# Optimization experiments

Measured on AMD Instinct MI355X. Metric: run time of the kernel, lower is better.

The kernel has to match this reference:

```python
import jax, jax.numpy as jnp
import numpy as np

V, E, H = 32000, 512, 1024
B, T = 32, 48
PAD = 0


def setup_inputs() -> dict:
    key = jax.random.key(0)
    ks = jax.random.split(key, 9)
    s = 0.05
    emb = jax.random.normal(ks[0], (V, E), jnp.float32) * s
    emb = emb.at[PAD].set(0.0)  # padding_idx row is zero in nn.Embedding
    return {
        "initial_hidden_state": jax.random.normal(ks[1], (B, H), jnp.float32),
        "target_sequence": jax.random.randint(ks[2], (B, T), 0, V),
        "emb": emb,
        "W_ih": jax.random.normal(ks[3], (3 * H, E), jnp.float32) * s,  # [r;z;n] input weights
        "W_hh": jax.random.normal(ks[4], (3 * H, H), jnp.float32) * s,
        "b_ih": jax.random.normal(ks[5], (3 * H,), jnp.float32) * s,
        "b_hh": jax.random.normal(ks[6], (3 * H,), jnp.float32) * s,
        "W_cls": jax.random.normal(ks[7], (V, H), jnp.float32) * s,
        "b_cls": jax.random.normal(ks[8], (V,), jnp.float32) * s,
    }


def _decode(initial_hidden_state, target_sequence, emb, W_ih, W_hh, b_ih, b_hh, W_cls, b_cls):
    # teacher forcing: sample_probability = 0.0 -> use_sample False
    idx_t = target_sequence.T  # [T, B]

    def step(h, y_idx):
        x = emb[y_idx]                                 # [B, E] embedding gather
        gi = x @ W_ih.T + b_ih                         # [B, 3H]
        gh = h @ W_hh.T + b_hh                         # [B, 3H]
        i_r, i_z, i_n = jnp.split(gi, 3, axis=-1)
        h_r, h_z, h_n = jnp.split(gh, 3, axis=-1)
        r = jax.nn.sigmoid(i_r + h_r)
        z = jax.nn.sigmoid(i_z + h_z)
        n = jnp.tanh(i_n + r * h_n)
        h_new = (1.0 - z) * n + z * h                  # torch GRUCell update
        score = h_new @ W_cls.T + b_cls                # [B, V]
        return h_new, score

    _, scores = jax.lax.scan(step, initial_hidden_state, idx_t)  # [T, B, V]
    return jnp.transpose(scores, (1, 0, 2))                      # [B, T, V]


def reference(initial_hidden_state, target_sequence, emb, W_ih, W_hh, b_ih, b_hh, W_cls, b_cls):
    return _decode(initial_hidden_state, target_sequence, emb, W_ih, W_hh, b_ih, b_hh, W_cls, b_cls)
```

## Files before the change

### kernel.cpp

```cpp
#include <hip/hip_runtime.h>
#include <hip/hip_bf16.h>

typedef __attribute__((ext_vector_type(8))) short short8;
typedef __attribute__((ext_vector_type(4))) float f32x4;
typedef __attribute__((ext_vector_type(4))) unsigned int u32x4;

#define T_STEPS 48
#define BATCH 32
#define EDIM 512
#define HDIM 1024
#define VOCAB 32000
#define GRU_BLOCKS 64
#define JPB 16
#define SENT 0x7FFF7FFFu
#define N_TILES 750
#define CNT_STRIDE 16
#define EARLY_WORKERS 128

#define HS_T_STRIDE 16384

__device__ __forceinline__ unsigned short f2bf(float f) {
    __hip_bfloat16 h = __float2bfloat16(f);
    return *reinterpret_cast<unsigned short*>(&h);
}
__device__ __forceinline__ float bf2f(unsigned short u) {
    union { unsigned int i; float f; } v;
    v.i = ((unsigned int)u) << 16;
    return v.f;
}

typedef __attribute__((address_space(1))) const void GAS;
typedef __attribute__((address_space(3))) void LAS;
__device__ __forceinline__ void gload_lds16(const unsigned short* g, unsigned short* l) {
    __builtin_amdgcn_global_load_lds((GAS*)g, (LAS*)(unsigned)(uintptr_t)l, 16, 0, 0);
}

__device__ __forceinline__ void store16_coh(unsigned int* p, u32x4 v) {
    asm volatile("global_store_dwordx4 %0, %1, off sc0 sc1"
                 :: "v"((unsigned long long)(uintptr_t)p), "v"(v) : "memory");
}

__global__ __launch_bounds__(256) void prep_kernel(
    const float* __restrict__ h0, const int* __restrict__ tseq,
    const float* __restrict__ emb, const float* __restrict__ w_ih,
    const float* __restrict__ w_hh, const float* __restrict__ w_cls,
    unsigned short* __restrict__ wcls_bf, unsigned short* __restrict__ wih_bf,
    unsigned short* __restrict__ whh_bf, unsigned short* __restrict__ x_bf,
    unsigned int* __restrict__ hs32, unsigned int* __restrict__ cnt8)
{
    const long R0 = (long)VOCAB * HDIM / 4;
    const long R1 = (long)3 * HDIM * EDIM / 4;
    const long R2 = (long)3 * HDIM * HDIM / 4;
    const long R3 = (long)T_STEPS * BATCH * EDIM / 4;
    const long R4 = (long)HS_T_STRIDE;
    const long R5 = (long)T_STEPS * HS_T_STRIDE / 4;
    const long R6 = 512;
    const long total = R0 + R1 + R2 + R3 + R4 + R5 + R6;

    for (long i = (long)blockIdx.x * blockDim.x + threadIdx.x; i < total;
         i += (long)gridDim.x * blockDim.x) {
        if (i < R0) {
            float4 v = reinterpret_cast<const float4*>(w_cls)[i];
            ushort4 u = { f2bf(v.x), f2bf(v.y), f2bf(v.z), f2bf(v.w) };
            *reinterpret_cast<ushort4*>(wcls_bf + i * 4) = u;
        } else if (i < R0 + R1) {
            long j = i - R0;
            float4 v = reinterpret_cast<const float4*>(w_ih)[j];
            ushort4 u = { f2bf(v.x), f2bf(v.y), f2bf(v.z), f2bf(v.w) };
            *reinterpret_cast<ushort4*>(wih_bf + j * 4) = u;
        } else if (i < R0 + R1 + R2) {
            long j = i - R0 - R1;
            float4 v = reinterpret_cast<const float4*>(w_hh)[j];
            ushort4 u = { f2bf(v.x), f2bf(v.y), f2bf(v.z), f2bf(v.w) };
            *reinterpret_cast<ushort4*>(whh_bf + j * 4) = u;
        } else if (i < R0 + R1 + R2 + R3) {
            long j = i - R0 - R1 - R2;
            int m = (int)(j >> 7);
            int kk4 = (int)(j & 127);
            int t = m >> 5, b = m & 31;
            int tok = tseq[b * T_STEPS + t];
            float4 v = reinterpret_cast<const float4*>(emb)[(long)tok * (EDIM / 4) + kk4];
            ushort4 u = { f2bf(v.x), f2bf(v.y), f2bf(v.z), f2bf(v.w) };
            *reinterpret_cast<ushort4*>(x_bf + (long)m * EDIM + kk4 * 4) = u;
        } else if (i < R0 + R1 + R2 + R3 + R4) {
            long j = i - R0 - R1 - R2 - R3;
            int w = (int)(j >> 5), b = (int)(j & 31);
            unsigned short a = f2bf(h0[b * HDIM + 2 * w]);
            unsigned short c = f2bf(h0[b * HDIM + 2 * w + 1]);
            hs32[j] = (unsigned)a | ((unsigned)c << 16);
        } else if (i < R0 + R1 + R2 + R3 + R4 + R5) {
            long j = i - R0 - R1 - R2 - R3 - R4;
            uint4 s = { SENT, SENT, SENT, SENT };
            reinterpret_cast<uint4*>(hs32 + HS_T_STRIDE)[j] = s;
        } else {
            long j = i - R0 - R1 - R2 - R3 - R4 - R5;
            uint4 z = { 0u, 0u, 0u, 0u };
            reinterpret_cast<uint4*>(cnt8)[j] = z;
        }
    }
}

__global__ __launch_bounds__(256) void gemm_gi(
    const unsigned short* __restrict__ A, const unsigned short* __restrict__ B,
    const float* __restrict__ bias, float* __restrict__ C, int K, int Ntot, int nM)
{
    const int nwg = gridDim.x;
    const int lin = blockIdx.x;
    const int q = nwg >> 3;
    const int wg = (lin & 7) * q + (lin >> 3);
    const int mi = wg % nM, ni = wg / nM;
    const int m0 = mi * 128, n0 = ni * 128;

    const int tid = threadIdx.x;
    const int lane = tid & 63;
    const int wid = tid >> 6;
    const int wr = wid >> 1, wc = wid & 1;

    __shared__ __align__(16) unsigned short As[128 * 32];
    __shared__ __align__(16) unsigned short Bs[128 * 32];

    f32x4 acc[4][4] = {};
    const int NT = K >> 5;
    const int srow = (lane >> 2);
    const int skk = (lane & 3) * 8;

    for (int kt = 0; kt < NT; ++kt) {
        __syncthreads();
        {
            const int kb = kt * 32;
#pragma unroll
            for (int h2 = 0; h2 < 2; ++h2) {
                const int i = wid + h2 * 4;
                const int row = i * 16 + srow;
                gload_lds16(A + (size_t)(m0 + row) * K + kb + skk, As + i * 512);
                gload_lds16(B + (size_t)(n0 + row) * K + kb + skk, Bs + i * 512);
            }
        }
        __syncthreads();

        const int kg = lane >> 4;
        const int l15 = lane & 15;
        short8 af[4], bf[4];
#pragma unroll
        for (int i = 0; i < 4; ++i) {
            af[i] = *(const short8*)(As + ((wr * 64 + i * 16 + l15) * 32 + kg * 8));
            bf[i] = *(const short8*)(Bs + ((wc * 64 + i * 16 + l15) * 32 + kg * 8));
        }
#pragma unroll
        for (int i = 0; i < 4; ++i)
#pragma unroll
            for (int j = 0; j < 4; ++j)
                acc[i][j] = __builtin_amdgcn_mfma_f32_16x16x32_bf16(af[i], bf[j], acc[i][j], 0, 0, 0);
    }

    const int l15 = lane & 15, lhi = lane >> 4;
#pragma unroll
    for (int i = 0; i < 4; ++i)
#pragma unroll
        for (int j = 0; j < 4; ++j) {
            int col = n0 + wc * 64 + j * 16 + l15;
            float bv = bias[col];
#pragma unroll
            for (int q2 = 0; q2 < 4; ++q2) {
                int row = m0 + wr * 64 + i * 16 + lhi * 4 + q2;
                C[(size_t)row * Ntot + col] = acc[i][j][q2] + bv;
            }
        }
}

__global__ __launch_bounds__(512, 1) void fused_kernel(
    unsigned int* __restrict__ hs32, unsigned int* __restrict__ hrow32,
    const unsigned short* __restrict__ whh_bf,
    const float* __restrict__ gi, const float* __restrict__ b_hh,
    const float* __restrict__ h0,
    const unsigned short* __restrict__ wcls_bf, const float* __restrict__ b_cls,
    float* __restrict__ out, unsigned int* __restrict__ cnt8,
    unsigned int* __restrict__ tileq)
{
    __shared__ __align__(16) char smem[124160];
    __shared__ unsigned short Hs[BATCH][JPB];
    __shared__ int sTile;

    const int tid = threadIdx.x;
    const int bid = blockIdx.x;
    const int lane = tid & 63, wid = tid >> 6;
    const int l15 = lane & 15, kg = lane >> 4;

    if (bid < GRU_BLOCKS) {
        unsigned short (*Wl)[1032] = reinterpret_cast<unsigned short (*)[1032]>(smem);
        float (*P)[32][49] = reinterpret_cast<float (*)[32][49]>(smem + 99072);

        const int j0 = bid * JPB;
        for (int c = tid; c < 48 * 128; c += 512) {
            int row = c >> 7, k8 = (c & 127) * 8;
            int g = row >> 4, jj = row & 15;
            *(short8*)&Wl[row][k8] =
                *(const short8*)(whh_bf + (size_t)(g * HDIM + j0 + jj) * HDIM + k8);
        }
        const int b = tid >> 4, jj = tid & 15;
        const int gj = j0 + jj;
        const float bhr = b_hh[gj];
        const float bhz = b_hh[HDIM + gj];
        const float bhn = b_hh[2 * HDIM + gj];
        float hloc = h0[b * HDIM + gj];
        __syncthreads();

        for (int t = 0; t < T_STEPS; ++t) {
            const size_t tb = (size_t)t * HS_T_STRIDE;
            const float* gr = gi + (size_t)(t * BATCH + b) * (3 * HDIM);
            float xr = gr[gj], xz = gr[HDIM + gj], xn = gr[2 * HDIM + gj];

            if (tid < 256) {
                if (t) {
                    const unsigned int* cp = cnt8 + (size_t)t * CNT_STRIDE + 2 * wid;
                    for (;;) {
                        unsigned ok = (lane < 2)
                            ? (__hip_atomic_load(cp + lane, __ATOMIC_RELAXED, __HIP_MEMORY_SCOPE_AGENT) >= 8u ? 1u : 0u)
                            : 1u;
                        if (__all(ok != 0u)) break;
                        __builtin_amdgcn_s_sleep(2);
                    }
                    asm volatile("" ::: "memory");
                }

                const int kq = wid * 256;
                unsigned wv[8][8];
#pragma unroll
                for (int ks = 0; ks < 8; ++ks) {
                    const int wbase = wid * 128 + ks * 16 + kg * 4;
#pragma unroll
                    for (int mi2 = 0; mi2 < 2; ++mi2) {
                        const int bb = mi2 * 16 + l15;
#pragma unroll
                        for (int q = 0; q < 4; ++q)
                            wv[ks][mi2 * 4 + q] = *(const unsigned*)(
                                hs32 + tb + (size_t)(wbase + q) * 32 + bb);
                    }
                }
                for (;;) {
                    int bad = 0;
#pragma unroll
                    for (int ks = 0; ks < 8; ++ks)
#pragma unroll
                        for (int i = 0; i < 8; ++i)
                            bad |= (wv[ks][i] == SENT);
                    if (!__any(bad)) break;
                    __builtin_amdgcn_s_sleep(1);
#pragma unroll
                    for (int ks = 0; ks < 8; ++ks)
#pragma unroll
                        for (int i = 0; i < 8; ++i)
                            if (wv[ks][i] == SENT) {
                                const int mi2 = i >> 2, q = i & 3;
                                wv[ks][i] = __hip_atomic_load(
                                    hs32 + tb + (size_t)(wid * 128 + ks * 16 + kg * 4 + q) * 32 + (mi2 * 16 + l15),
                                    __ATOMIC_RELAXED, __HIP_MEMORY_SCOPE_AGENT);
                            }
                }
                f32x4 acc[2][3] = {};
#pragma unroll
                for (int ks = 0; ks < 8; ++ks) {
                    const int kb = kq + ks * 32 + kg * 8;
                    union U8 { unsigned u[4]; short8 s; };
                    short8 ah[2];
#pragma unroll
                    for (int mi2 = 0; mi2 < 2; ++mi2) {
                        U8 x;
#pragma unroll
                        for (int q = 0; q < 4; ++q) x.u[q] = wv[ks][mi2 * 4 + q];
                        ah[mi2] = x.s;
                    }
#pragma unroll
                    for (int fr = 0; fr < 3; ++fr) {
                        short8 bh = *(const short8*)&Wl[fr * 16 + l15][kb];
#pragma unroll
                        for (int mi2 = 0; mi2 < 2; ++mi2)
                            acc[mi2][fr] = __builtin_amdgcn_mfma_f32_16x16x32_bf16(ah[mi2], bh, acc[mi2][fr], 0, 0, 0);
                    }
                }
#pragma unroll
                for (int mi2 = 0; mi2 < 2; ++mi2)
#pragma unroll
                    for (int fr = 0; fr < 3; ++fr)
#pragma unroll
                        for (int q = 0; q < 4; ++q)
                            P[wid][mi2 * 16 + kg * 4 + q][fr * 16 + l15] = acc[mi2][fr][q];
            }
            __syncthreads();

            {
                float ghr = 0.f, ghz = 0.f, ghn = 0.f;
#pragma unroll
                for (int w = 0; w < 4; ++w) {
                    ghr += P[w][b][jj];
                    ghz += P[w][b][16 + jj];
                    ghn += P[w][b][32 + jj];
                }
                float r = 1.f / (1.f + __expf(-(xr + ghr + bhr)));
                float z = 1.f / (1.f + __expf(-(xz + ghz + bhz)));
                float n = tanhf(xn + r * (ghn + bhn));
                float hnew = (1.f - z) * n + z * hloc;
                hloc = hnew;
                Hs[b][jj] = f2bf(hnew);
            }
            __syncthreads();

            if (tid < 64) {
                const int q = tid >> 3, c = tid & 7;
                u32x4 d;
#pragma unroll
                for (int w2 = 0; w2 < 4; ++w2) {
                    int bb = c * 4 + w2;
                    d[w2] = (unsigned)Hs[bb][2 * q] | ((unsigned)Hs[bb][2 * q + 1] << 16);
                }
                store16_coh(hs32 + (size_t)(t + 1) * HS_T_STRIDE + (size_t)((j0 >> 1) + q) * 32 + c * 4, d);
            } else if (tid < 128) {
                const int i = tid - 64, bb = i >> 1, half = i & 1;
                u32x4 d;
#pragma unroll
                for (int w2 = 0; w2 < 4; ++w2) {
                    int q = half * 4 + w2;
                    d[w2] = (unsigned)Hs[bb][2 * q] | ((unsigned)Hs[bb][2 * q + 1] << 16);
                }
                store16_coh(hrow32 + ((size_t)t * BATCH + bb) * 512 + (j0 >> 1) + half * 4, d);
            }
            __syncthreads();
            if (tid == 0)
                __hip_atomic_fetch_add(cnt8 + (size_t)(t + 1) * CNT_STRIDE + (bid >> 3), 1u,
                                       __ATOMIC_RELAXED, __HIP_MEMORY_SCOPE_AGENT);
        }
    } else if (bid >= GRU_BLOCKS + EARLY_WORKERS) {
        if (wid == 0) {
            const unsigned int* cp = cnt8 + (size_t)T_STEPS * CNT_STRIDE;
            for (;;) {
                unsigned v = (lane < 8)
                    ? __hip_atomic_load(cp + lane, __ATOMIC_RELAXED, __HIP_MEMORY_SCOPE_AGENT)
                    : 8u;
                if (__all(v >= 8u)) break;
                __builtin_amdgcn_s_sleep(64);
            }
        }
        __syncthreads();
    }

    const unsigned short* hrowA = (const unsigned short*)hrow32;
    const int srow = lane >> 2;
    const int skk = (lane & 3) * 8;
    const int wm = wid >> 1, wn = wid & 1;

    unsigned short* As0 = (unsigned short*)(smem);
    unsigned short* Bs0 = (unsigned short*)(smem + 16384);
    unsigned short* As1 = (unsigned short*)(smem + 32768);
    unsigned short* Bs1 = (unsigned short*)(smem + 49152);

    for (;;) {
        __syncthreads();
        if (tid == 0)
            sTile = (int)__hip_atomic_fetch_add(tileq, 1u, __ATOMIC_RELAXED, __HIP_MEMORY_SCOPE_AGENT);
        __syncthreads();
        const int k = sTile;
        if (k >= N_TILES) break;
        const int mi = k / 125, ni = k - mi * 125;
        const int m0 = mi * 256, n0 = ni * 256;

        {
            if (wid == 0) {
                const unsigned int* cp = cnt8 + (size_t)(mi * 8 + 8) * CNT_STRIDE;
                for (;;) {
                    unsigned v = (lane < 8)
                        ? __hip_atomic_load(cp + lane, __ATOMIC_RELAXED, __HIP_MEMORY_SCOPE_AGENT)
                        : 8u;
                    if (__all(v >= 8u)) break;
                    __builtin_amdgcn_s_sleep(32);
                }
            }
            __syncthreads();
            asm volatile("" ::: "memory");
        }

        f32x4 acc[4][8] = {};

#define STAGE(KT, AB, BB)                                                      \
        {                                                                      \
            const int kb = (KT) * 32;                                          \
            _Pragma("unroll")                                                  \
            for (int h2 = 0; h2 < 2; ++h2) {                                   \
                const int i = wid + h2 * 8;                                    \
                const int row = i * 16 + srow;                                 \
                gload_lds16(hrowA + (size_t)(m0 + row) * HDIM + kb + skk, (AB) + i * 512); \
                gload_lds16(wcls_bf + (size_t)(n0 + row) * HDIM + kb + skk, (BB) + i * 512); \
            }                                                                  \
        }
#define COMPUTE(AB, BB)                                                        \
        {                                                                      \
            short8 af[4], bf[8];                                               \
            _Pragma("unroll")                                                  \
            for (int i = 0; i < 4; ++i)                                        \
                af[i] = *(const short8*)((AB) + ((wm * 64 + i * 16 + l15) * 32 + kg * 8)); \
            _Pragma("unroll")                                                  \
            for (int j = 0; j < 8; ++j)                                        \
                bf[j] = *(const short8*)((BB) + ((wn * 128 + j * 16 + l15) * 32 + kg * 8)); \
            _Pragma("unroll")                                                  \
            for (int i = 0; i < 4; ++i)                                        \
                _Pragma("unroll")                                              \
                for (int j = 0; j < 8; ++j)                                    \
                    acc[i][j] = __builtin_amdgcn_mfma_f32_16x16x32_bf16(af[i], bf[j], acc[i][j], 0, 0, 0); \
        }

        STAGE(0, As0, Bs0);
        __syncthreads();
        for (int it = 0; it < 16; ++it) {
            const int kt0 = 2 * it;
            STAGE(kt0 + 1, As1, Bs1);
            COMPUTE(As0, Bs0);
            __syncthreads();
            if (kt0 + 2 < 32) STAGE(kt0 + 2, As0, Bs0);
            COMPUTE(As1, Bs1);
            __syncthreads();
        }
#undef STAGE
#undef COMPUTE

        const int lhi = lane >> 4;
#pragma unroll
        for (int i = 0; i < 4; ++i)
#pragma unroll
            for (int j = 0; j < 8; ++j) {
                int col = n0 + wn * 128 + j * 16 + l15;
                float bv = b_cls[col];
#pragma unroll
                for (int q2 = 0; q2 < 4; ++q2) {
                    int row = m0 + wm * 64 + i * 16 + lhi * 4 + q2;
                    int t = row >> 5, bb = row & 31;
                    __builtin_nontemporal_store(acc[i][j][q2] + bv,
                        &out[(size_t)(bb * T_STEPS + t) * VOCAB + col]);
                }
            }
    }
}

extern "C" void kernel_launch(void* const* d_in, const int* in_sizes, int n_in,
                              void* d_out, int out_size, void* d_ws, size_t ws_size,
                              hipStream_t stream) {
    const float* h0    = (const float*)d_in[0];
    const int*   tseq  = (const int*)d_in[1];
    const float* emb   = (const float*)d_in[2];
    const float* w_ih  = (const float*)d_in[3];
    const float* w_hh  = (const float*)d_in[4];
    const float* b_ih  = (const float*)d_in[5];
    const float* b_hh  = (const float*)d_in[6];
    const float* w_cls = (const float*)d_in[7];
    const float* b_cls = (const float*)d_in[8];
    float* out = (float*)d_out;

    char* w = (char*)d_ws;
    unsigned short* wcls_bf = (unsigned short*)w; w += (size_t)VOCAB * HDIM * 2;
    unsigned short* wih_bf  = (unsigned short*)w; w += (size_t)3 * HDIM * EDIM * 2;
    unsigned short* whh_bf  = (unsigned short*)w; w += (size_t)3 * HDIM * HDIM * 2;
    unsigned short* x_bf    = (unsigned short*)w; w += (size_t)T_STEPS * BATCH * EDIM * 2;
    unsigned int*   hs32    = (unsigned int*)w;   w += (size_t)(T_STEPS + 1) * HS_T_STRIDE * 4;
    unsigned int*   hrow32  = (unsigned int*)w;   w += (size_t)T_STEPS * BATCH * 512 * 4;
    float* gi               = (float*)w;          w += (size_t)T_STEPS * BATCH * 3 * HDIM * 4;
    unsigned int* cnt8      = (unsigned int*)w;   w += 8192;
    unsigned int* tileq     = cnt8 + 1024;

    prep_kernel<<<2048, 256, 0, stream>>>(h0, tseq, emb, w_ih, w_hh, w_cls,
                                          wcls_bf, wih_bf, whh_bf, x_bf, hs32, cnt8);

    gemm_gi<<<(T_STEPS * BATCH / 128) * (3 * HDIM / 128), 256, 0, stream>>>(
        x_bf, wih_bf, b_ih, gi, EDIM, 3 * HDIM, T_STEPS * BATCH / 128);

    fused_kernel<<<256, 512, 0, stream>>>(hs32, hrow32, whh_bf, gi, b_hh, h0,
                                          wcls_bf, b_cls, out, cnt8, tileq);
}
```

Baseline: 345.7 us.

## Split last M-block into half-height tiles to balance classifier GEMM tail

The classifier GEMM's final row block (the last 256 rows of h, which wait on the latest GRU steps) is now covered by 128x256 tiles instead of 256x256 ones, making 250 small tiles after the 625 big ones. The smaller tiles use a separate 4x2 warp layout with their own staging and LDS offsets. This is meant to shrink the tail that runs after the recurrence finishes and spread it over more workgroups. The early-worker count also drops from 128 to 96. The cost is extra code size and more register pressure from two code paths, plus lower per-tile reuse for the last block.

Result: no change. 343.2 us, median of 2 (-0.7%).

```diff
diff --git a/kernel.cpp b/kernel.cpp
--- a/kernel.cpp
+++ b/kernel.cpp
@@ -13,9 +13,10 @@
 #define GRU_BLOCKS 64
 #define JPB 16
 #define SENT 0x7FFF7FFFu
-#define N_TILES 750
+#define N_BIG 625
+#define N_TILES 875
 #define CNT_STRIDE 16
-#define EARLY_WORKERS 128
+#define EARLY_WORKERS 96
 
 #define HS_T_STRIDE 16384
 
@@ -346,12 +347,6 @@
     const unsigned short* hrowA = (const unsigned short*)hrow32;
     const int srow = lane >> 2;
     const int skk = (lane & 3) * 8;
-    const int wm = wid >> 1, wn = wid & 1;
-
-    unsigned short* As0 = (unsigned short*)(smem);
-    unsigned short* Bs0 = (unsigned short*)(smem + 16384);
-    unsigned short* As1 = (unsigned short*)(smem + 32768);
-    unsigned short* Bs1 = (unsigned short*)(smem + 49152);
 
     for (;;) {
         __syncthreads();
@@ -360,8 +355,10 @@
         __syncthreads();
         const int k = sTile;
         if (k >= N_TILES) break;
-        const int mi = k / 125, ni = k - mi * 125;
-        const int m0 = mi * 256, n0 = ni * 256;
+
+        int mi, m0, n0, big;
+        if (k < N_BIG) { mi = k / 125; n0 = (k - mi * 125) * 256; m0 = mi * 256; big = 1; }
+        else { int idx = k - N_BIG; mi = 5; m0 = 1280 + (idx & 1) * 128; n0 = (idx >> 1) * 256; big = 0; }
 
         {
             if (wid == 0) {
@@ -378,64 +375,135 @@
             asm volatile("" ::: "memory");
         }
 
-        f32x4 acc[4][8] = {};
+        if (big) {
+            const int wm = wid >> 1, wn = wid & 1;
+            unsigned short* As0 = (unsigned short*)(smem);
+            unsigned short* Bs0 = (unsigned short*)(smem + 16384);
+            unsigned short* As1 = (unsigned short*)(smem + 32768);
+            unsigned short* Bs1 = (unsigned short*)(smem + 49152);
+            f32x4 acc[4][8] = {};
 
 #define STAGE(KT, AB, BB)                                                      \
-        {                                                                      \
-            const int kb = (KT) * 32;                                          \
-            _Pragma("unroll")                                                  \
-            for (int h2 = 0; h2 < 2; ++h2) {                                   \
-                const int i = wid + h2 * 8;                                    \
-                const int row = i * 16 + srow;                                 \
-                gload_lds16(hrowA + (size_t)(m0 + row) * HDIM + kb + skk, (AB) + i * 512); \
-                gload_lds16(wcls_bf + (size_t)(n0 + row) * HDIM + kb + skk, (BB) + i * 512); \
-            }                                                                  \
-        }
+            {                                                                  \
+                const int kb = (KT) * 32;                                      \
+                _Pragma("unroll")                                              \
+                for (int h2 = 0; h2 < 2; ++h2) {                               \
+                    const int i = wid + h2 * 8;                                \
+                    const int row = i * 16 + srow;                             \
+                    gload_lds16(hrowA + (size_t)(m0 + row) * HDIM + kb + skk, (AB) + i * 512); \
+                    gload_lds16(wcls_bf + (size_t)(n0 + row) * HDIM + kb + skk, (BB) + i * 512); \
+                }                                                              \
+            }
 #define COMPUTE(AB, BB)                                                        \
-        {                                                                      \
-            short8 af[4], bf[8];                                               \
-            _Pragma("unroll")                                                  \
-            for (int i = 0; i < 4; ++i)                                        \
-                af[i] = *(const short8*)((AB) + ((wm * 64 + i * 16 + l15) * 32 + kg * 8)); \
-            _Pragma("unroll")                                                  \
-            for (int j = 0; j < 8; ++j)                                        \
-                bf[j] = *(const short8*)((BB) + ((wn * 128 + j * 16 + l15) * 32 + kg * 8)); \
-            _Pragma("unroll")                                                  \
-            for (int i = 0; i < 4; ++i)                                        \
+            {                                                                  \
+                short8 af[4], bf[8];                                           \
+                _Pragma("unroll")                                              \
+                for (int i = 0; i < 4; ++i)                                    \
+                    af[i] = *(const short8*)((AB) + ((wm * 64 + i * 16 + l15) * 32 + kg * 8)); \
                 _Pragma("unroll")                                              \
                 for (int j = 0; j < 8; ++j)                                    \
-                    acc[i][j] = __builtin_amdgcn_mfma_f32_16x16x32_bf16(af[i], bf[j], acc[i][j], 0, 0, 0); \
-        }
-
-        STAGE(0, As0, Bs0);
-        __syncthreads();
-        for (int it = 0; it < 16; ++it) {
-            const int kt0 = 2 * it;
-            STAGE(kt0 + 1, As1, Bs1);
-            COMPUTE(As0, Bs0);
+                    bf[j] = *(const short8*)((BB) + ((wn * 128 + j * 16 + l15) * 32 + kg * 8)); \
+                _Pragma("unroll")                                              \
+                for (int i = 0; i < 4; ++i)                                    \
+                    _Pragma("unroll")                                          \
+                    for (int j = 0; j < 8; ++j)                                \
+                        acc[i][j] = __builtin_amdgcn_mfma_f32_16x16x32_bf16(af[i], bf[j], acc[i][j], 0, 0, 0); \
+            }
+            STAGE(0, As0, Bs0);
             __syncthreads();
-            if (kt0 + 2 < 32) STAGE(kt0 + 2, As0, Bs0);
-            COMPUTE(As1, Bs1);
-            __syncthreads();
-        }
+            for (int it = 0; it < 16; ++it) {
+                const int kt0 = 2 * it;
+                STAGE(kt0 + 1, As1, Bs1);
+                COMPUTE(As0, Bs0);
+                __syncthreads();
+                if (kt0 + 2 < 32) STAGE(kt0 + 2, As0, Bs0);
+                COMPUTE(As1, Bs1);
+                __syncthreads();
+            }
 #undef STAGE
 #undef COMPUTE
-
-        const int lhi = lane >> 4;
-#pragma unroll
-        for (int i = 0; i < 4; ++i)
-#pragma unroll
-            for (int j = 0; j < 8; ++j) {
-                int col = n0 + wn * 128 + j * 16 + l15;
-                float bv = b_cls[col];
-#pragma unroll
-                for (int q2 = 0; q2 < 4; ++q2) {
-                    int row = m0 + wm * 64 + i * 16 + lhi * 4 + q2;
-                    int t = row >> 5, bb = row & 31;
-                    __builtin_nontemporal_store(acc[i][j][q2] + bv,
-                        &out[(size_t)(bb * T_STEPS + t) * VOCAB + col]);
-                }
-            }
+            const int lhi = lane >> 4;
+#pragma unroll
+            for (int i = 0; i < 4; ++i)
+#pragma unroll
+                for (int j = 0; j < 8; ++j) {
+                    int col = n0 + wn * 128 + j * 16 + l15;
+                    float bv = b_cls[col];
+#pragma unroll
+                    for (int q2 = 0; q2 < 4; ++q2) {
+                        int row = m0 + wm * 64 + i * 16 + lhi * 4 + q2;
+                        int t = row >> 5, bb = row & 31;
+                        __builtin_nontemporal_store(acc[i][j][q2] + bv,
+                            &out[(size_t)(bb * T_STEPS + t) * VOCAB + col]);
+                    }
+                }
+        } else {
+            const int wm = wid >> 2, wn = wid & 3;
+            unsigned short* As0 = (unsigned short*)(smem);
+            unsigned short* Bs0 = (unsigned short*)(smem + 8192);
+            unsigned short* As1 = (unsigned short*)(smem + 24576);
+            unsigned short* Bs1 = (unsigned short*)(smem + 32768);
+            f32x4 acc[4][4] = {};
+
+#define STAGE1(KT, AB, BB)                                                     \
+            {                                                                  \
+                const int kb = (KT) * 32;                                      \
+                _Pragma("unroll")                                              \
+                for (int h2 = 0; h2 < 3; ++h2) {                               \
+                    const int c = wid * 3 + h2;                     \
+                    if (c < 8) {                                               \
+                        const int row = c * 16 + srow;                         \
+                        gload_lds16(hrowA + (size_t)(m0 + row) * HDIM + kb + skk, (AB) + c * 512); \
+                    } else {                                                   \
+                        const int row = (c - 8) * 16 + srow;                   \
+                        gload_lds16(wcls_bf + (size_t)(n0 + row) * HDIM + kb + skk, (BB) + (c - 8) * 512); \
+                    }                                                          \
+                }                                                              \
+            }
+#define COMPUTE1(AB, BB)                                                       \
+            {                                                                  \
+                short8 af[4], bf[4];                                           \
+                _Pragma("unroll")                                              \
+                for (int i = 0; i < 4; ++i)                                    \
+                    af[i] = *(const short8*)((AB) + ((wm * 64 + i * 16 + l15) * 32 + kg * 8)); \
+                _Pragma("unroll")                                              \
+                for (int j = 0; j < 4; ++j)                                    \
+                    bf[j] = *(const short8*)((BB) + ((wn * 64 + j * 16 + l15) * 32 + kg * 8)); \
+                _Pragma("unroll")                                              \
+                for (int i = 0; i < 4; ++i)                                    \
+                    _Pragma("unroll")                                          \
+                    for (int j = 0; j < 4; ++j)                                \
+                        acc[i][j] = __builtin_amdgcn_mfma_f32_16x16x32_bf16(af[i], bf[j], acc[i][j], 0, 0, 0); \
+            }
+            STAGE1(0, As0, Bs0);
+            __syncthreads();
+            for (int it = 0; it < 16; ++it) {
+                const int kt0 = 2 * it;
+                STAGE1(kt0 + 1, As1, Bs1);
+                COMPUTE1(As0, Bs0);
+                __syncthreads();
+                if (kt0 + 2 < 32) STAGE1(kt0 + 2, As0, Bs0);
+                COMPUTE1(As1, Bs1);
+                __syncthreads();
+            }
+#undef STAGE1
+#undef COMPUTE1
+            const int lhi = lane >> 4;
+#pragma unroll
+            for (int i = 0; i < 4; ++i)
+#pragma unroll
+                for (int j = 0; j < 4; ++j) {
+                    int col = n0 + wn * 64 + j * 16 + l15;
+                    float bv = b_cls[col];
+#pragma unroll
+                    for (int q2 = 0; q2 < 4; ++q2) {
+                        int row = m0 + wm * 64 + i * 16 + lhi * 4 + q2;
+                        int t = row >> 5, bb = row & 31;
+                        __builtin_nontemporal_store(acc[i][j][q2] + bv,
+                            &out[(size_t)(bb * T_STEPS + t) * VOCAB + col]);
+                    }
+                }
+        }
     }
 }
 
```
